# Kernel optimization log

Hardware: AMD Instinct MI355X
Metric: run time of the kernel (lower is better)

Reference implementation:

```python
import jax, jax.numpy as jnp
import numpy as np

B, T, C, H = 4, 1024, 1024, 16
D = C // H          # head size 64
CH = 64             # chunk size (min(T,64))
NK = T // CH        # number of key chunks
TOPK = 32           # sparse_topk
SCALE = 1.0 / np.sqrt(D)


def setup_inputs() -> dict:
    key = jax.random.key(0)
    ks = jax.random.split(key, 7)
    x = jax.random.normal(ks[0], (B, T, C), dtype=jnp.float32)
    importance_scores = jax.random.normal(ks[1], (B, T, H), dtype=jnp.float32)
    temperatures = jax.random.uniform(ks[2], (B, H), dtype=jnp.float32)
    Wq = jax.random.normal(ks[3], (C, C), dtype=jnp.float32) * 0.02
    Wk = jax.random.normal(ks[4], (C, C), dtype=jnp.float32) * 0.02
    Wv = jax.random.normal(ks[5], (C, C), dtype=jnp.float32) * 0.02
    Wo = jax.random.normal(ks[6], (C, C), dtype=jnp.float32) * 0.02
    return {"x": x, "importance_scores": importance_scores,
            "temperatures": temperatures, "Wq": Wq, "Wk": Wk, "Wv": Wv, "Wo": Wo}


def reference(x, importance_scores, temperatures, Wq, Wk, Wv, Wo):
    # projections (eval mode: all dropouts are identity)
    q = jnp.nan_to_num(x @ Wq, nan=0.0, posinf=1.0, neginf=-1.0)
    q = q.reshape(B, T, H, D).transpose(0, 2, 1, 3)            # [B,H,T,D]
    k = (x @ Wk).reshape(B, T, H, D).transpose(0, 2, 1, 3)     # [B,H,T,D]
    v = (x @ Wv).reshape(B, T, H, D).transpose(0, 2, 1, 3)
    k_ch = k.reshape(B, H, NK, CH, D)                          # key chunks
    v_ch = v.reshape(B, H, NK, CH, D)

    # scores per (query, key-chunk, in-chunk-key): [B,H,T,NK,CH]
    scores = jnp.einsum('bhqd,bhkcd->bhqkc', q, k_ch) * SCALE
    temp = jnp.clip(temperatures, 0.1, 100.0)[:, :, None, None, None]
    scores = scores / temp

    # sigmoid importance gating (per query position, broadcast over keys)
    imp = jax.nn.sigmoid(importance_scores.transpose(0, 2, 1))  # [B,H,T]
    mask_weight = jax.nn.sigmoid((imp - 0.5) * 10.0)[:, :, :, None, None]
    scores = scores * mask_weight

    # per-chunk top-k filtering (keep scores >= k-th largest, zero the rest)
    top_scores = jax.lax.top_k(scores, TOPK)[0]
    thr = top_scores[..., -1:]
    scores = scores * (scores >= thr).astype(scores.dtype)

    # per-key-chunk softmax (stable, denom clamped), as in the torch loop
    m = jnp.max(scores, axis=-1, keepdims=True)
    e = jnp.exp(scores - m)
    denom = jnp.clip(jnp.sum(e, axis=-1, keepdims=True), 1e-6, None)
    p = e / denom                                               # [B,H,T,NK,CH]

    out = jnp.einsum('bhqkc,bhkcd->bhqd', p, v_ch)              # sum over chunks
    normalizer = jnp.clip(jnp.sum(p, axis=(3, 4)), 1e-6, None)  # [B,H,T]
    out = out / normalizer[..., None]
    out = jnp.nan_to_num(out, nan=0.0, posinf=1.0, neginf=-1.0)

    out = out.transpose(0, 2, 1, 3).reshape(B, T, C)
    return out @ Wo
```

## Files before the change

### kernel.cpp

```cpp
#include <hip/hip_runtime.h>
#include <stdint.h>

typedef _Float16 f16;
typedef _Float16 f16x8 __attribute__((ext_vector_type(8)));
typedef _Float16 f16x4 __attribute__((ext_vector_type(4)));
typedef float f32x4 __attribute__((ext_vector_type(4)));
typedef unsigned uint2v __attribute__((ext_vector_type(2)));

#define AS1 __attribute__((address_space(1)))
#define AS3 __attribute__((address_space(3)))

#if __has_builtin(__builtin_amdgcn_exp2f)
#define EXP2(x) __builtin_amdgcn_exp2f(x)
#else
#define EXP2(x) exp2f(x)
#endif

__device__ __forceinline__ void gl_lds16(const void* g, void* l) {
  __builtin_amdgcn_global_load_lds((const AS1 uint32_t*)g, (AS3 uint32_t*)l, 16, 0, 0);
}

__device__ __forceinline__ unsigned quadsum_u(unsigned v) {
  unsigned a = v, b = v;
  asm("s_nop 1\n\tv_permlane16_swap_b32 %0, %1" : "+v"(a), "+v"(b));
  unsigned s = a + b;
  unsigned a2 = s, b2 = s;
  asm("s_nop 1\n\tv_permlane32_swap_b32 %0, %1" : "+v"(a2), "+v"(b2));
  return a2 + b2;
}
__device__ __forceinline__ float quadsum_f(float v) {
  float a = v, b = v;
  asm("s_nop 1\n\tv_permlane16_swap_b32 %0, %1" : "+v"(a), "+v"(b));
  float s = a + b;
  float a2 = s, b2 = s;
  asm("s_nop 1\n\tv_permlane32_swap_b32 %0, %1" : "+v"(a2), "+v"(b2));
  return a2 + b2;
}

__device__ __forceinline__ unsigned pk_cnt_ge(unsigned k, unsigned cm1, unsigned ones) {
  unsigned d;
  asm("v_pk_sub_u16 %0, %1, %2 clamp" : "=v"(d) : "v"(k), "v"(cm1));
  asm("v_pk_min_u16 %0, %1, %2" : "=v"(d) : "v"(d), "v"(ones));
  return d;
}

__device__ __forceinline__ unsigned cvt_pk_u32(float a, float b) {
  return __builtin_bit_cast(unsigned, __builtin_amdgcn_cvt_pkrtz(a, b));
}

__global__ void k_prep(const float* __restrict__ x,
                       const float* __restrict__ Wq, const float* __restrict__ Wk,
                       const float* __restrict__ Wv, const float* __restrict__ Wo,
                       f16* __restrict__ xh,
                       f16* __restrict__ Wqt, f16* __restrict__ Wkt,
                       f16* __restrict__ Wvt, f16* __restrict__ Wot) {
  __shared__ __align__(16) f16 lt[64][72];
  const int t = threadIdx.x;
  if (blockIdx.z == 4) {
    int bid2 = blockIdx.y * 16 + blockIdx.x;
    #pragma unroll 4
    for (int it = 0; it < 16; ++it) {
      int i = ((bid2 * 16 + it) * 256 + t) * 4;
      float4 v = *(const float4*)(x + i);
      f16x4 o = { (f16)v.x, (f16)v.y, (f16)v.z, (f16)v.w };
      *(f16x4*)(xh + i) = o;
    }
    return;
  }
  const float* src; f16* dst; float scl;
  switch (blockIdx.z) {
    case 0: src = Wq; dst = Wqt; scl = 1.0f; break;
    case 1: src = Wk; dst = Wkt; scl = 1.0f; break;
    case 2: src = Wv; dst = Wvt; scl = 1.0f; break;
    default: src = Wo; dst = Wot; scl = 0.0625f; break;
  }
  int n0 = blockIdx.x * 64, k0 = blockIdx.y * 64;
  int kk = t >> 4;
  int nn = (t & 15) * 4;
  #pragma unroll
  for (int p = 0; p < 4; ++p) {
    int k = kk + p * 16;
    float4 v = *(const float4*)(src + (size_t)(k0 + k) * 1024 + n0 + nn);
    lt[nn + 0][k] = (f16)(v.x * scl);
    lt[nn + 1][k] = (f16)(v.y * scl);
    lt[nn + 2][k] = (f16)(v.z * scl);
    lt[nn + 3][k] = (f16)(v.w * scl);
  }
  __syncthreads();
  int row = t >> 2;
  int kp = (t & 3) * 16;
  f16* d = dst + (size_t)(n0 + row) * 1024 + k0 + kp;
  *(f16x8*)d       = *(const f16x8*)&lt[row][kp];
  *(f16x8*)(d + 8) = *(const f16x8*)&lt[row][kp + 8];
}

template<int MODE, int TM>
__global__ __launch_bounds__(256, 3)
void k_gemm(const f16* __restrict__ A, const f16* __restrict__ Bt0,
            const f16* __restrict__ A2, const f16* __restrict__ Bt2,
            const f16* __restrict__ Bt1,
            void* __restrict__ out0, void* __restrict__ out1, void* __restrict__ out2) {
  constexpr int SMEM_MAIN = TM * 64 * 2 + 128 * 64 * 2;
  constexpr int SMEM_EP = (MODE == 0) ? 4 * 64 * 72 * 2 : 0;
  constexpr int SMEM_SZ = SMEM_EP > SMEM_MAIN ? SMEM_EP : SMEM_MAIN;
  __shared__ __align__(16) char smem[SMEM_SZ];
  f16* As = (f16*)smem;
  f16* Bs = (f16*)(smem + TM * 64 * 2);
  f16* EPb = (f16*)smem;
  const int n0 = blockIdx.x * 128, m0 = blockIdx.y * TM;
  const int tid = threadIdx.x, wave = tid >> 6, lane = tid & 63;
  const int l15 = lane & 15, quad = lane >> 4;
  const int wm = (wave >> 1) * (TM / 2), wn = (wave & 1) * 64;
  constexpr int NI = TM / 32;
  constexpr int PA = TM / 32;
  const f16* Bsrc = Bt0;
  int nb = n0;
  if (MODE == 0) {
    if (n0 >= 2048)      { Bsrc = Bt2; nb = n0 - 2048; }
    else if (n0 >= 1024) { Bsrc = Bt1; nb = n0 - 1024; }
  }
  f32x4 acc[NI][4] = {};
  const int sr = lane >> 3, sg = lane & 7;
  const int gl = sg ^ sr;
  const f16* ap[PA];
  const f16* ap2[PA];
  const f16* bp[4];
  #pragma unroll
  for (int p = 0; p < PA; ++p) {
    size_t off = (size_t)(m0 + wave * (TM / 4) + p * 8 + sr) * 1024 + gl * 8;
    ap[p] = A + off;
    if (MODE == 2) ap2[p] = A2 + off;
  }
  #pragma unroll
  for (int p = 0; p < 4; ++p)
    bp[p] = Bsrc + (size_t)(nb + wave * 32 + p * 8 + sr) * 1024 + gl * 8;

  for (int kt = 0; kt < 16; ++kt) {
    __syncthreads();
    #pragma unroll
    for (int p = 0; p < PA; ++p) {
      if (MODE == 2) {
        f16x8 a0 = *(const f16x8*)ap[p];
        f16x8 a1 = *(const f16x8*)ap2[p];
        *(f16x8*)&As[(wave * (TM / 4) + p * 8) * 64 + lane * 8] = a0 + a1;
        ap2[p] += 64;
      } else {
        gl_lds16(ap[p], &As[(wave * (TM / 4) + p * 8) * 64]);
      }
      ap[p] += 64;
    }
    #pragma unroll
    for (int p = 0; p < 4; ++p) {
      gl_lds16(bp[p], &Bs[(wave * 32 + p * 8) * 64]);
      bp[p] += 64;
    }
    __syncthreads();
    #pragma unroll
    for (int ks = 0; ks < 2; ++ks) {
      f16x8 af[NI], bf[4];
      #pragma unroll
      for (int i = 0; i < NI; ++i) {
        int row = wm + i * 16 + l15;
        int g2 = (ks * 4 + quad) ^ (row & 7);
        af[i] = *(const f16x8*)&As[row * 64 + g2 * 8];
      }
      #pragma unroll
      for (int j = 0; j < 4; ++j) {
        int row = wn + j * 16 + l15;
        int g2 = (ks * 4 + quad) ^ (row & 7);
        bf[j] = *(const f16x8*)&Bs[row * 64 + g2 * 8];
      }
      #pragma unroll
      for (int i = 0; i < NI; ++i)
        #pragma unroll
        for (int j = 0; j < 4; ++j)
          acc[i][j] = __builtin_amdgcn_mfma_f32_16x16x32_f16(af[i], bf[j], acc[i][j], 0, 0, 0);
    }
  }

  if (MODE == 0) {
    if (n0 < 2048) {
      __syncthreads();
      f16* ep = &EPb[wave * 64 * 72];
      #pragma unroll
      for (int i = 0; i < NI; ++i)
        #pragma unroll
        for (int j = 0; j < 4; ++j)
          #pragma unroll
          for (int r = 0; r < 4; ++r)
            ep[(i * 16 + quad * 4 + r) * 72 + j * 16 + l15] = (f16)acc[i][j][r];
      f16* dst = (n0 < 1024) ? (f16*)out0 : (f16*)out1;
      const int hh = ((n0 + wn) & 1023) >> 6;
      const int r8 = lane >> 3, cg = lane & 7;
      #pragma unroll
      for (int it = 0; it < 8; ++it) {
        int row = it * 8 + r8;
        f16x8 vv = *(const f16x8*)&ep[row * 72 + cg * 8];
        int m = m0 + wm + row;
        int b = m >> 10, t = m & 1023;
        *(f16x8*)&dst[(size_t)((b * 16 + hh) * 1024 + t) * 64 + cg * 8] = vv;
      }
    } else {
      #pragma unroll
      for (int i = 0; i < NI; ++i)
        #pragma unroll
        for (int j = 0; j < 4; ++j) {
          int mb = m0 + wm + i * 16 + quad * 4;
          int b = mb >> 10, t = mb & 1023;
          int n = n0 + wn + j * 16 + l15;
          int nn2 = n & 1023, hh = nn2 >> 6, d = nn2 & 63;
          f16x4 vv = { (f16)acc[i][j][0], (f16)acc[i][j][1], (f16)acc[i][j][2], (f16)acc[i][j][3] };
          *(f16x4*)((f16*)out2 + ((size_t)(b * 16 + hh) * 64 + d) * 1024 + t) = vv;
        }
    }
  } else {
    #pragma unroll
    for (int i = 0; i < NI; ++i)
      #pragma unroll
      for (int j = 0; j < 4; ++j)
        #pragma unroll
        for (int r = 0; r < 4; ++r) {
          int m = m0 + wm + i * 16 + quad * 4 + r;
          int n = n0 + wn + j * 16 + l15;
          ((float*)out0)[(size_t)m * 1024 + n] = acc[i][j][r];
        }
  }
}

__global__ __launch_bounds__(256, 5)
void k_attn(const f16* __restrict__ Q16, const f16* __restrict__ K16, const f16* __restrict__ Vt16,
            const float* __restrict__ imp, const float* __restrict__ temps,
            f16* __restrict__ part0, f16* __restrict__ part1) {
  __shared__ __align__(16) f16 Qs[64 * 64];
  __shared__ __align__(16) f16 Ks[64 * 64];
  __shared__ __align__(16) f16 Vs[64 * 64];
  __shared__ __align__(16) f16 Ps[64 * 64];

  const int bid = blockIdx.x & 1023;
  const int half = blockIdx.x >> 10;
  const int b = bid >> 8, h = (bid >> 4) & 15, qt = bid & 15;
  const int bh = b * 16 + h;
  const int tid = threadIdx.x, wave = tid >> 6, lane = tid & 63;
  const int l15 = lane & 15, quad = lane >> 4;

  float sc = (0.125f * 1.44269504088896340736f) / fminf(fmaxf(temps[bh], 0.1f), 100.0f);
  const int tq = qt * 64 + wave * 16 + l15;
  float is = imp[(size_t)(b * 1024 + tq) * 16 + h];
  float s1 = 1.0f / (1.0f + __expf(-is));
  float mwv = 1.0f / (1.0f + __expf(-(s1 - 0.5f) * 10.0f));
  const float rs = sc * mwv;

  const unsigned vones = 0x00010001u;

  const int sr = lane >> 3, sg = lane & 7;
  const int gls = sg ^ sr;
  const size_t qoff = ((size_t)bh * 1024 + qt * 64) * 64;
  gl_lds16(Q16 + qoff + (size_t)(wave * 16 + sr) * 64 + gls * 8,     &Qs[(wave * 16) * 64]);
  gl_lds16(Q16 + qoff + (size_t)(wave * 16 + 8 + sr) * 64 + gls * 8, &Qs[(wave * 16 + 8) * 64]);

  const size_t kbase = (size_t)bh * 1024 * 64;
  const size_t vbase = (size_t)bh * 64 * 1024;
  const f16* kp0 = K16 + kbase + (size_t)(half * 512 + wave * 16 + sr) * 64 + gls * 8;
  const f16* kp1 = kp0 + 8 * 64;
  const f16* vp0 = Vt16 + vbase + (size_t)(wave * 16 + sr) * 1024 + half * 512 + gls * 8;
  const f16* vp1 = vp0 + 8 * 1024;
  f16* lk0 = &Ks[(wave * 16) * 64];
  f16* lk1 = &Ks[(wave * 16 + 8) * 64];
  f16* lv0 = &Vs[(wave * 16) * 64];
  f16* lv1 = &Vs[(wave * 16 + 8) * 64];

  const int mrow = wave * 16 + l15;
  f16* pst[4];
  #pragma unroll
  for (int j = 0; j < 4; ++j)
    pst[j] = &Ps[mrow * 64 + (((j * 2 + (quad >> 1)) ^ (l15 & 7)) * 8 + (quad & 1) * 4)];

  f32x4 oacc[4] = {};

  for (int ck = 0; ck < 8; ++ck) {
    __syncthreads();
    gl_lds16(kp0, lk0); gl_lds16(kp1, lk1);
    gl_lds16(vp0, lv0); gl_lds16(vp1, lv1);
    kp0 += 4096; kp1 += 4096; vp0 += 64; vp1 += 64;
    __syncthreads();

    f32x4 sacc[4] = {};
    #pragma unroll
    for (int ks = 0; ks < 2; ++ks) {
      int qr = wave * 16 + l15;
      int gq = (ks * 4 + quad) ^ (qr & 7);
      f16x8 bq = *(const f16x8*)&Qs[qr * 64 + gq * 8];
      #pragma unroll
      for (int j = 0; j < 4; ++j) {
        int kr = j * 16 + l15;
        int gk = (ks * 4 + quad) ^ (kr & 7);
        f16x8 ak = *(const f16x8*)&Ks[kr * 64 + gk * 8];
        sacc[j] = __builtin_amdgcn_mfma_f32_16x16x32_f16(ak, bq, sacc[j], 0, 0, 0);
      }
    }

    float xx[4][4];
    #pragma unroll
    for (int j = 0; j < 4; ++j)
      #pragma unroll
      for (int r = 0; r < 4; ++r)
        xx[j][r] = __builtin_amdgcn_fmed3f(__builtin_fmaf(sacc[j][r], rs, 192.0f), 132.0f, 252.0f);

    unsigned pk16[8];
    #pragma unroll
    for (int j = 0; j < 4; ++j) {
      unsigned a0 = __builtin_bit_cast(unsigned, xx[j][0]) >> 10;
      unsigned a1 = __builtin_bit_cast(unsigned, xx[j][1]) >> 10;
      unsigned a2 = __builtin_bit_cast(unsigned, xx[j][2]) >> 10;
      unsigned a3 = __builtin_bit_cast(unsigned, xx[j][3]) >> 10;
      pk16[j * 2 + 0] = __builtin_amdgcn_perm(a1, a0, 0x05040100);
      pk16[j * 2 + 1] = __builtin_amdgcn_perm(a3, a2, 0x05040100);
    }

    unsigned tkp = 0xC000C000u;
    #pragma unroll
    for (int bit = 12; bit >= 0; --bit) {
      const unsigned cand = tkp | ((1u << bit) | (1u << (bit + 16)));
      const unsigned cm1 = cand - 0x00010001u;
      unsigned acc = 0;
      #pragma unroll
      for (int i = 0; i < 8; ++i)
        acc += pk_cnt_ge(pk16[i], cm1, vones);
      unsigned q = quadsum_u(acc);
      unsigned tot2 = q + (q << 16);
      tkp = (tot2 >= (32u << 16)) ? cand : tkp;
    }
    const unsigned tk32 = 0x43000000u | ((tkp & 0x1fffu) << 10);

    float e[4][4];
    #pragma unroll
    for (int j = 0; j < 4; ++j)
      #pragma unroll
      for (int r = 0; r < 4; ++r) {
        float sel = (__builtin_bit_cast(unsigned, xx[j][r]) >= tk32) ? xx[j][r] : 192.0f;
        e[j][r] = EXP2(sel - 192.0f);
      }
    float dsum = ((e[0][0] + e[0][1]) + (e[0][2] + e[0][3]))
               + ((e[1][0] + e[1][1]) + (e[1][2] + e[1][3]))
               + ((e[2][0] + e[2][1]) + (e[2][2] + e[2][3]))
               + ((e[3][0] + e[3][1]) + (e[3][2] + e[3][3]));
    dsum = quadsum_f(dsum);
    const float dinv = __builtin_amdgcn_rcpf(dsum);

    #pragma unroll
    for (int j = 0; j < 4; ++j) {
      uint2v pw = { cvt_pk_u32(e[j][0] * dinv, e[j][1] * dinv),
                    cvt_pk_u32(e[j][2] * dinv, e[j][3] * dinv) };
      *(f16x4*)pst[j] = __builtin_bit_cast(f16x4, pw);
    }

    #pragma unroll
    for (int ks = 0; ks < 2; ++ks) {
      int row = wave * 16 + l15;
      int g2 = (ks * 4 + quad) ^ (row & 7);
      f16x8 ap2 = *(const f16x8*)&Ps[row * 64 + g2 * 8];
      #pragma unroll
      for (int j = 0; j < 4; ++j) {
        int rn = j * 16 + l15;
        int gn = (ks * 4 + quad) ^ (rn & 7);
        f16x8 bv = *(const f16x8*)&Vs[rn * 64 + gn * 8];
        oacc[j] = __builtin_amdgcn_mfma_f32_16x16x32_f16(ap2, bv, oacc[j], 0, 0, 0);
      }
    }
  }

  f16* pd = half ? part1 : part0;
  #pragma unroll
  for (int j = 0; j < 4; ++j)
    #pragma unroll
    for (int r = 0; r < 4; ++r) {
      int m = wave * 16 + quad * 4 + r;
      int t = qt * 64 + m;
      int d = j * 16 + l15;
      pd[(size_t)(b * 1024 + t) * 1024 + h * 64 + d] = (f16)oacc[j][r];
    }
}

extern "C" void kernel_launch(void* const* d_in, const int* in_sizes, int n_in,
                              void* d_out, int out_size, void* d_ws, size_t ws_size,
                              hipStream_t stream) {
  (void)in_sizes; (void)n_in; (void)out_size; (void)ws_size;
  const float* x     = (const float*)d_in[0];
  const float* imp   = (const float*)d_in[1];
  const float* temps = (const float*)d_in[2];
  const float* Wq    = (const float*)d_in[3];
  const float* Wk    = (const float*)d_in[4];
  const float* Wv    = (const float*)d_in[5];
  const float* Wo    = (const float*)d_in[6];
  float* out = (float*)d_out;

  char* w = (char*)d_ws;
  f16* xh   = (f16*)w; w += (size_t)4096 * 1024 * 2;
  f16* Wqt  = (f16*)w; w += (size_t)1024 * 1024 * 2;
  f16* Wkt  = (f16*)w; w += (size_t)1024 * 1024 * 2;
  f16* Wvt  = (f16*)w; w += (size_t)1024 * 1024 * 2;
  f16* Wot  = (f16*)w; w += (size_t)1024 * 1024 * 2;
  f16* Q16  = (f16*)w; w += (size_t)4096 * 1024 * 2;
  f16* K16  = (f16*)w; w += (size_t)4096 * 1024 * 2;
  f16* Vt16 = (f16*)w; w += (size_t)4096 * 1024 * 2;
  f16* O16  = (f16*)w; w += (size_t)4096 * 1024 * 2;

  k_prep<<<dim3(16, 16, 5), dim3(256), 0, stream>>>(x, Wq, Wk, Wv, Wo, xh, Wqt, Wkt, Wvt, Wot);
  k_gemm<0, 128><<<dim3(24, 32), dim3(256), 0, stream>>>(xh, Wqt, nullptr, Wvt, Wkt,
                                                         (void*)Q16, (void*)K16, (void*)Vt16);
  k_attn<<<dim3(2048), dim3(256), 0, stream>>>(Q16, K16, Vt16, imp, temps, xh, O16);
  k_gemm<2, 64><<<dim3(8, 64), dim3(256), 0, stream>>>(xh, Wot, O16, nullptr, nullptr,
                                                       (void*)out, nullptr, nullptr);
}
```

Baseline: 234.6 us.

## Double-buffer K/V tiles in attention kernel and remap block order

Adds two LDS buffers for the K and V chunks so the next chunk's global-to-LDS loads are issued before computing on the current one. Explicit vmcnt waits replace the double __syncthreads. Block indices are also permuted so consecutive blocks are strided by 8, which may change L2/XCD locality. Occupancy hint drops from 5 to 3 because LDS use grows.

```diff
diff --git a/kernel.cpp b/kernel.cpp
--- a/kernel.cpp
+++ b/kernel.cpp
@@ -227,17 +227,18 @@
   }
 }
 
-__global__ __launch_bounds__(256, 5)
+__global__ __launch_bounds__(256, 3)
 void k_attn(const f16* __restrict__ Q16, const f16* __restrict__ K16, const f16* __restrict__ Vt16,
             const float* __restrict__ imp, const float* __restrict__ temps,
             f16* __restrict__ part0, f16* __restrict__ part1) {
   __shared__ __align__(16) f16 Qs[64 * 64];
-  __shared__ __align__(16) f16 Ks[64 * 64];
-  __shared__ __align__(16) f16 Vs[64 * 64];
+  __shared__ __align__(16) f16 KsB[2][64 * 64];
+  __shared__ __align__(16) f16 VsB[2][64 * 64];
   __shared__ __align__(16) f16 Ps[64 * 64];
 
-  const int bid = blockIdx.x & 1023;
-  const int half = blockIdx.x >> 10;
+  const int orig = ((int)blockIdx.x & 7) * 256 + ((int)blockIdx.x >> 3);
+  const int bid = orig & 1023;
+  const int half = orig >> 10;
   const int b = bid >> 8, h = (bid >> 4) & 15, qt = bid & 15;
   const int bh = b * 16 + h;
   const int tid = threadIdx.x, wave = tid >> 6, lane = tid & 63;
@@ -264,10 +265,12 @@
   const f16* kp1 = kp0 + 8 * 64;
   const f16* vp0 = Vt16 + vbase + (size_t)(wave * 16 + sr) * 1024 + half * 512 + gls * 8;
   const f16* vp1 = vp0 + 8 * 1024;
-  f16* lk0 = &Ks[(wave * 16) * 64];
-  f16* lk1 = &Ks[(wave * 16 + 8) * 64];
-  f16* lv0 = &Vs[(wave * 16) * 64];
-  f16* lv1 = &Vs[(wave * 16 + 8) * 64];
+
+  gl_lds16(kp0, &KsB[0][(wave * 16) * 64]);
+  gl_lds16(kp1, &KsB[0][(wave * 16 + 8) * 64]);
+  gl_lds16(vp0, &VsB[0][(wave * 16) * 64]);
+  gl_lds16(vp1, &VsB[0][(wave * 16 + 8) * 64]);
+  kp0 += 4096; kp1 += 4096; vp0 += 64; vp1 += 64;
 
   const int mrow = wave * 16 + l15;
   f16* pst[4];
@@ -278,11 +281,23 @@
   f32x4 oacc[4] = {};
 
   for (int ck = 0; ck < 8; ++ck) {
-    __syncthreads();
-    gl_lds16(kp0, lk0); gl_lds16(kp1, lk1);
-    gl_lds16(vp0, lv0); gl_lds16(vp1, lv1);
-    kp0 += 4096; kp1 += 4096; vp0 += 64; vp1 += 64;
-    __syncthreads();
+    const int cur = ck & 1, nxt = cur ^ 1;
+    __builtin_amdgcn_s_barrier();
+    if (ck < 7) {
+      gl_lds16(kp0, &KsB[nxt][(wave * 16) * 64]);
+      gl_lds16(kp1, &KsB[nxt][(wave * 16 + 8) * 64]);
+      gl_lds16(vp0, &VsB[nxt][(wave * 16) * 64]);
+      gl_lds16(vp1, &VsB[nxt][(wave * 16 + 8) * 64]);
+      kp0 += 4096; kp1 += 4096; vp0 += 64; vp1 += 64;
+      asm volatile("s_waitcnt vmcnt(4)" ::: "memory");
+    } else {
+      asm volatile("s_waitcnt vmcnt(0)" ::: "memory");
+    }
+    __builtin_amdgcn_sched_barrier(0);
+    __builtin_amdgcn_s_barrier();
+
+    const f16* Kc = &KsB[cur][0];
+    const f16* Vc = &VsB[cur][0];
 
     f32x4 sacc[4] = {};
     #pragma unroll
@@ -294,7 +309,7 @@
       for (int j = 0; j < 4; ++j) {
         int kr = j * 16 + l15;
         int gk = (ks * 4 + quad) ^ (kr & 7);
-        f16x8 ak = *(const f16x8*)&Ks[kr * 64 + gk * 8];
+        f16x8 ak = *(const f16x8*)&Kc[kr * 64 + gk * 8];
         sacc[j] = __builtin_amdgcn_mfma_f32_16x16x32_f16(ak, bq, sacc[j], 0, 0, 0);
       }
     }
@@ -363,7 +378,7 @@
       for (int j = 0; j < 4; ++j) {
         int rn = j * 16 + l15;
         int gn = (ks * 4 + quad) ^ (rn & 7);
-        f16x8 bv = *(const f16x8*)&Vs[rn * 64 + gn * 8];
+        f16x8 bv = *(const f16x8*)&Vc[rn * 64 + gn * 8];
         oacc[j] = __builtin_amdgcn_mfma_f32_16x16x32_f16(ap2, bv, oacc[j], 0, 0, 0);
       }
     }
```

Result: faster. 224.7 us (-4.2%).
